# Kernel tuning notes

Hardware: AMD Instinct MI355X
Metric: run time of the kernel (lower is better)

Reference implementation:

```python
import jax, jax.numpy as jnp
import numpy as np
from jax import lax

B, S, D, STEPS, OUT = 512, 256, 256, 256, 3


def setup_inputs() -> dict:
    key = jax.random.key(0)
    ks = jax.random.split(key, 16)
    sc = 0.05
    n = lambda k, shp: jax.random.normal(k, shp, jnp.float32) * sc
    return {
        "e_all": jax.random.normal(ks[0], (B, S, D), jnp.float32),
        "e_last": jax.random.normal(ks[1], (1, B, D), jnp.float32),
        # NN_Attention params
        "Wa": n(ks[2], (D, D)), "ba": n(ks[3], (D,)),
        "Ua": n(ks[4], (D, D)), "bu": n(ks[5], (D,)),
        "Va": n(ks[6], (D,)), "bv": n(ks[7], ()),
        # GRU params (PyTorch layout: W_ih [3D, 3+D], W_hh [3D, D])
        "W_ih": n(ks[8], (3 * D, D + 3)), "b_ih": n(ks[9], (3 * D,)),
        "W_hh": n(ks[10], (3 * D, D)), "b_hh": n(ks[11], (3 * D,)),
        # output linear D -> 3
        "Wo": n(ks[12], (OUT, D)), "bo": n(ks[13], (OUT,)),
    }


def _decode(e_all, e_last, Wa, ba, Ua, bu, Va, bv, W_ih, b_ih, W_hh, b_hh, Wo, bo):
    # Ua(keys) is constant across steps -> precompute once (same math)
    Ua_keys = jnp.einsum('bsd,ed->bse', e_all, Ua) + bu  # [B, S, D]

    def step(carry, _):
        h, x_in = carry
        # Bahdanau attention: Va(tanh(Wa(q) + Ua(keys)))
        q = h @ Wa.T + ba                                       # [B, D]
        scores = jnp.einsum('bsd,d->bs', jnp.tanh(q[:, None, :] + Ua_keys), Va) + bv
        w = jax.nn.softmax(scores, axis=-1)                     # [B, S]
        ctx = jnp.einsum('bs,bsd->bd', w, e_all)                # [B, D]
        # GRU cell on input [context ; d_input] (cat order matches torch code)
        x = jnp.concatenate([ctx, x_in], axis=-1)               # [B, D+3]
        gi = x @ W_ih.T + b_ih
        gh = h @ W_hh.T + b_hh
        i_r, i_z, i_n = jnp.split(gi, 3, axis=-1)
        h_r, h_z, h_n = jnp.split(gh, 3, axis=-1)
        r = jax.nn.sigmoid(i_r + h_r)
        z = jax.nn.sigmoid(i_z + h_z)
        nn_ = jnp.tanh(i_n + r * h_n)
        h_new = (1.0 - z) * nn_ + z * h
        out = h_new @ Wo.T + bo                                 # [B, 3]
        return (h_new, out), (out, w)

    h0 = e_last[0]                                              # [B, D]
    x0 = jnp.zeros((h0.shape[0], OUT), h0.dtype)
    (hT, _), (outs, ws) = lax.scan(step, (h0, x0), None, length=STEPS)
    d_outputs = outs.transpose(1, 0, 2)                         # [B, STEPS, 3]
    cross_attn = ws.transpose(1, 0, 2).reshape(h0.shape[0], 1, STEPS * S)
    return d_outputs, hT[None], cross_attn


def reference(e_all, e_last, Wa, ba, Ua, bu, Va, bv, W_ih, b_ih, W_hh, b_hh, Wo, bo):
    return _decode(e_all, e_last, Wa, ba, Ua, bu, Va, bv, W_ih, b_ih, W_hh, b_hh, Wo, bo)
```

## Files before the change

kernel.cpp:

```cpp
#include <hip/hip_runtime.h>
#include <hip/hip_bf16.h>
#include <stdint.h>

#define NB 512
#define NS 256
#define ND 256
#define NT 256
#define NO 3

#define LOG2E 1.44269504088896340736f
#define C2 (2.0f*LOG2E)

typedef float f32x2 __attribute__((ext_vector_type(2)));

#if __has_builtin(__builtin_amdgcn_exp2f)
__device__ __forceinline__ float exp2_fast(float x){ return __builtin_amdgcn_exp2f(x); }
#else
__device__ __forceinline__ float exp2_fast(float x){ return exp2f(x); }
#endif
#if __has_builtin(__builtin_amdgcn_rcpf)
__device__ __forceinline__ float rcp_fast(float x){ return __builtin_amdgcn_rcpf(x); }
#else
__device__ __forceinline__ float rcp_fast(float x){ return 1.0f/x; }
#endif
// ... 100 lines not shown
  __shared__ float At[ND][20];
  const int t = threadIdx.x;
  const int m0 = blockIdx.x * 16;
  const int b  = m0 >> 8;
  const int s0 = m0 & (NS-1);
  #pragma unroll
  for (int i=0;i<16;i++)
    At[t][i] = e_all[(size_t)(m0+i)*ND + t];
  __syncthreads();
  float acc[16];
  float bue = bu[t];
  #pragma unroll
  for (int i=0;i<16;i++) acc[i] = bue;
  for (int d=0; d<ND; ++d){
    float u = UaT[d*ND + t];
    const float4 a0 = *(const float4*)&At[d][0];
    const float4 a1 = *(const float4*)&At[d][4];
    const float4 a2 = *(const float4*)&At[d][8];
    const float4 a3 = *(const float4*)&At[d][12];
    acc[0]+=a0.x*u;  acc[1]+=a0.y*u;  acc[2]+=a0.z*u;  acc[3]+=a0.w*u;
    acc[4]+=a1.x*u;  acc[5]+=a1.y*u;  acc[6]+=a1.z*u;  acc[7]+=a1.w*u;
    acc[8]+=a2.x*u;  acc[9]+=a2.y*u;  acc[10]+=a2.z*u; acc[11]+=a2.w*u;
    acc[12]+=a3.x*u; acc[13]+=a3.y*u; acc[14]+=a3.z*u; acc[15]+=a3.w*u;
  }
  const int e16 = t>>4, j = t&15;
  uint8_t* base = UKQ + (((size_t)b*16 + e16)*256 + s0)*16 + j;
  #pragma unroll
  for (int i=0;i<16;i++){
    uint32_t mine = enc_e4m3(acc[i] * C2);
    uint32_t other = (uint32_t)__shfl_xor((int)mine, 1);
    if (!(t & 1))
      *(uint16_t*)(base + (size_t)i*16) = (uint16_t)(mine | (other << 8));
  }
}

__global__ void k_epq(const float* __restrict__ e_all, uint32_t* __restrict__ EPQ){
  int idx = blockIdx.x*256 + threadIdx.x;
  if (idx >= NB*64*256) return;
  int d  = idx & 255;
  int s4 = (idx >> 8) & 63;
  int b  = idx >> 14;
  const float* e = e_all + ((size_t)b*NS + 4*s4)*ND + d;
  uint32_t v = (uint32_t)enc_e4m3(e[0])
             | ((uint32_t)enc_e4m3(e[ND])   << 8)
             | ((uint32_t)enc_e4m3(e[2*ND]) << 16)
             | ((uint32_t)enc_e4m3(e[3*ND]) << 24);
  EPQ[idx] = v;
}

__global__ void k_wh(const float* __restrict__ Wa, const float* __restrict__ W_hh,
                     uint4* __restrict__ WH){
  int idx = blockIdx.x*256 + threadIdx.x;
  if (idx >= 128*256) return;
  int d = idx & 255, k2 = idx >> 8;
  uint4 v;
  v.x = pack2(Wa  [(size_t)d*256       + 2*k2], Wa  [(size_t)d*256       + 2*k2+1]);
  v.y = pack2(W_hh[(size_t)d*256       + 2*k2], W_hh[(size_t)d*256       + 2*k2+1]);
  v.z = pack2(W_hh[(size_t)(256+d)*256 + 2*k2], W_hh[(size_t)(256+d)*256 + 2*k2+1]);
  v.w = pack2(W_hh[(size_t)(512+d)*256 + 2*k2], W_hh[(size_t)(512+d)*256 + 2*k2+1]);
  WH[idx] = v;
}

__global__ void k_wx(const float* __restrict__ W_ih, uint32_t* __restrict__ WX){
  int idx = blockIdx.x*256 + threadIdx.x;
  if (idx >= 132*256) return;
  int d = idx & 255, k2 = idx >> 8;
  float r0=0,r1=0,z0=0,z1=0,n0=0,n1=0;
  int ka = 2*k2, kb = 2*k2+1;
  if (ka < 259){
    r0 = W_ih[(size_t)d*259       + ka];
    z0 = W_ih[(size_t)(256+d)*259 + ka];
    n0 = W_ih[(size_t)(512+d)*259 + ka];
  }
  if (kb < 259){
    r1 = W_ih[(size_t)d*259       + kb];
    z1 = W_ih[(size_t)(256+d)*259 + kb];
    n1 = W_ih[(size_t)(512+d)*259 + kb];
  }
  WX[(size_t)idx*3+0] = pack2(r0,r1);
  WX[(size_t)idx*3+1] = pack2(z0,z1);
  WX[(size_t)idx*3+2] = pack2(n0,n1);
}

__global__ void __launch_bounds__(1024, 4) k_decode(
    const uint8_t* __restrict__ UKQ, const uint32_t* __restrict__ EPQ,
    const uint4* __restrict__ WH, const uint32_t* __restrict__ WX,
    const float* __restrict__ e_last,
    const float* __restrict__ Va, const float* __restrict__ bv,
    const float* __restrict__ b_ih, const float* __restrict__ b_hh,
    const float* __restrict__ ba, const float* __restrict__ bo,
    const float* __restrict__ Wo,
    float* __restrict__ dout, float* __restrict__ hT_out, float* __restrict__ ca)
{
  __shared__ __align__(16) uint8_t  ukl[65536];
  __shared__ __align__(16) uint32_t epl[16384];
  __shared__ __align__(16) float    scr[16][ND];
  __shared__ float    ghp[3][ND];
  __shared__ float    hf[ND];
  __shared__ float    xin[4];
  __shared__ uint32_t xb[260];
  __shared__ __align__(16) float qL[ND];
  __shared__ __align__(16) float va2[ND];
  __shared__ float    WoL[3*ND];
  __shared__ __align__(16) float wl[NS];
  __shared__ float    red[8];

  const int t    = threadIdx.x;
  const int d    = t & 255;
  const int q4   = t >> 8;
  const int lane = t & 63;
  const int w    = t >> 6;
  const int b0   = blockIdx.x * 2;

  if (q4 == 0){
    va2[d] = 2.0f*Va[d];
    WoL[d] = Wo[d]; WoL[256+d] = Wo[256+d]; WoL[512+d] = Wo[512+d];
  }
  const float bias_r  = b_ih[d]     + b_hh[d];
  const float bias_z  = b_ih[256+d] + b_hh[256+d];
  const float bias_ni = b_ih[512+d];
  const float bias_nh = b_hh[512+d];
  const float ba_d = ba[d];
  const float bv0  = bv[0];
  const float bo0 = bo[0], bo1 = bo[1], bo2 = bo[2];
  __syncthreads();
  float sumVaQ = 0.f;
  {
    #pragma unroll 8
    for (int e = q4*64; e < q4*64+64; ++e) sumVaQ += va2[e];
    sumVaQ *= 0.5f;
  }

  #pragma unroll 1
  for (int r=0; r<2; ++r){
    const int b = b0 + r;

    {
      const uint4* srcU = (const uint4*)(UKQ + (size_t)b*65536);
      uint4* dstU = (uint4*)ukl;
      #pragma unroll
      for (int i=0;i<4;i++) dstU[t + i*1024] = srcU[t + i*1024];
      const uint4* srcE = (const uint4*)(EPQ + (size_t)b*16384);
      uint4* dstE = (uint4*)epl;
      #pragma unroll
      for (int i=0;i<4;i++) dstE[t + i*1024] = srcE[t + i*1024];
    }
    if (q4 == 0){
      hf[d] = e_last[(size_t)b*ND + d];
      if (d < 4) xin[d] = 0.f;
    }
    __syncthreads();
    if (t < 128) xb[130+t] = pack2(hf[2*t], hf[2*t+1]);
    if (t == 128){ xb[128]=0u; xb[129]=0u; xb[258]=0u; xb[259]=0u; }
    __syncthreads();

    float* ca_b = ca   + (size_t)b*(NT*NS);
    float* do_b = dout + (size_t)b*(NT*NO);

    #pragma unroll 1
    for (int step=0; step<NT; ++step){
      {
        float aq=0.f, ar=0.f, az=0.f, an=0.f;
        const uint4* wh = WH + (size_t)(q4*32)*256 + d;
        const uint32_t* xh = &xb[130 + q4*32];
        #pragma unroll 1
        for (int kk=0; kk<32; kk+=4){
          uint4 w0 = wh[(size_t)(kk+0)*256];
          uint4 w1 = wh[(size_t)(kk+1)*256];
          uint4 w2 = wh[(size_t)(kk+2)*256];
          uint4 w3 = wh[(size_t)(kk+3)*256];
          uint32_t x0 = xh[kk+0], x1 = xh[kk+1], x2 = xh[kk+2], x3 = xh[kk+3];
          aq=dot2bf(w0.x,x0,aq); ar=dot2bf(w0.y,x0,ar); az=dot2bf(w0.z,x0,az); an=dot2bf(w0.w,x0,an);
          aq=dot2bf(w1.x,x1,aq); ar=dot2bf(w1.y,x1,ar); az=dot2bf(w1.z,x1,az); an=dot2bf(w1.w,x1,an);
          aq=dot2bf(w2.x,x2,aq); ar=dot2bf(w2.y,x2,ar); az=dot2bf(w2.z,x2,az); an=dot2bf(w2.w,x2,an);
          aq=dot2bf(w3.x,x3,aq); ar=dot2bf(w3.y,x3,ar); az=dot2bf(w3.z,x3,az); an=dot2bf(w3.w,x3,an);
        }
        scr[q4*4+0][d]=aq; scr[q4*4+1][d]=ar; scr[q4*4+2][d]=az; scr[q4*4+3][d]=an;
      }
      __syncthreads();
      if (q4 == 0){
        qL[d]     = ((scr[0][d]+scr[4][d]) + (scr[8][d]+scr[12][d]) + ba_d) * C2;
        ghp[0][d] =  (scr[1][d]+scr[5][d]) + (scr[9][d]+scr[13][d]);
        ghp[1][d] =  (scr[2][d]+scr[6][d]) + (scr[10][d]+scr[14][d]);
        ghp[2][d] =  (scr[3][d]+scr[7][d]) + (scr[11][d]+scr[15][d]);
      }
      __syncthreads();

      {
        float acc = 0.f;
        #pragma unroll
        for (int j=0;j<4;j++){
          uint4 u = *(const uint4*)(ukl + (size_t)(q4*4+j)*4096 + d*16);
          const float* qb = &qL[q4*64 + j*16];
          const float* vb = &va2[q4*64 + j*16];
          acc = s_dword(u.x, *(const float4*)&qb[0],  *(const float4*)&vb[0],  acc);
          acc = s_dword(u.y, *(const float4*)&qb[4],  *(const float4*)&vb[4],  acc);
          acc = s_dword(u.z, *(const float4*)&qb[8],  *(const float4*)&vb[8],  acc);
          acc = s_dword(u.w, *(const float4*)&qb[12], *(const float4*)&vb[12], acc);
        }
        scr[q4][d] = sumVaQ - acc;
      }
      __syncthreads();

      float p_reg = 0.f;
      if (q4 == 0){
        float sc = (scr[0][d]+scr[1][d]) + (scr[2][d]+scr[3][d]) + bv0;
        p_reg = exp2_fast(sc * LOG2E);
        float ssum = p_reg;
        #pragma unroll
        for (int o=32;o;o>>=1) ssum += __shfl_xor(ssum, o);
        if (lane==0) red[w] = ssum;
      }
      __syncthreads();
      if (q4 == 0){
        float ssum = (red[0]+red[1]) + (red[2]+red[3]);
        float wgt = p_reg * rcp_fast(ssum);
        __builtin_nontemporal_store(wgt, &ca_b[(size_t)step*NS + d]);
        wl[d] = wgt;
      }
      __syncthreads();

      {
        float c0=0,c1=0,c2=0,c3=0;
        #pragma unroll
        for (int i=0;i<4;i++){
          int s4 = w*4 + i;
          uint4 ev = *(const uint4*)(epl + (size_t)s4*256 + lane*4);
          float4 w4 = *(const float4*)&wl[s4*4];
          c0 = c_dword(ev.x, w4, c0);
          c1 = c_dword(ev.y, w4, c1);
          c2 = c_dword(ev.z, w4, c2);
          c3 = c_dword(ev.w, w4, c3);
        }
        *(float4*)&scr[w][lane*4] = make_float4(c0,c1,c2,c3);
      }
      __syncthreads();
      if (q4 == 0){
        float cx = 0.f;
        #pragma unroll
        for (int i=0;i<16;i++) cx += scr[i][d];
        float other = __shfl_xor(cx, 1);
        if (!(d&1)) xb[d>>1] = pack2(cx, other);
        if (d==128) xb[128] = pack2(xin[0], xin[1]);
        if (d==129) xb[129] = pack2(xin[2], 0.f);
      }
      __syncthreads();

      {
        float ar=0.f, az=0.f, an=0.f;
        const int k0 = q4*33;
        const uint32_t* wx = WX + ((size_t)k0*256 + d)*3;
        #pragma unroll 1
        for (int kk=0; kk<32; kk+=4){
          const uint32_t* p0 = wx + (size_t)(kk+0)*768;
          const uint32_t* p1 = wx + (size_t)(kk+1)*768;
          const uint32_t* p2 = wx + (size_t)(kk+2)*768;
          const uint32_t* p3 = wx + (size_t)(kk+3)*768;
          uint32_t r0=p0[0], z0=p0[1], n0=p0[2];
          uint32_t r1=p1[0], z1=p1[1], n1=p1[2];
          uint32_t r2=p2[0], z2=p2[1], n2=p2[2];
          uint32_t r3=p3[0], z3=p3[1], n3=p3[2];
          uint32_t x0 = xb[k0+kk+0], x1 = xb[k0+kk+1];
          uint32_t x2 = xb[k0+kk+2], x3 = xb[k0+kk+3];
          ar=dot2bf(r0,x0,ar); az=dot2bf(z0,x0,az); an=dot2bf(n0,x0,an);
          ar=dot2bf(r1,x1,ar); az=dot2bf(z1,x1,az); an=dot2bf(n1,x1,an);
          ar=dot2bf(r2,x2,ar); az=dot2bf(z2,x2,az); an=dot2bf(n2,x2,an);
          ar=dot2bf(r3,x3,ar); az=dot2bf(z3,x3,az); an=dot2bf(n3,x3,an);
        }
        {
          const uint32_t* p = wx + (size_t)32*768;
          uint32_t xa = xb[k0+32];
          ar=dot2bf(p[0],xa,ar); az=dot2bf(p[1],xa,az); an=dot2bf(p[2],xa,an);
        }
        scr[q4*3+0][d]=ar; scr[q4*3+1][d]=az; scr[q4*3+2][d]=an;
      }
      __syncthreads();
      if (q4 == 0){
        float ar  = (scr[0][d]+scr[3][d]) + (scr[6][d]+scr[9][d])  + ghp[0][d] + bias_r;
        float az  = (scr[1][d]+scr[4][d]) + (scr[7][d]+scr[10][d]) + ghp[1][d] + bias_z;
        float ani = (scr[2][d]+scr[5][d]) + (scr[8][d]+scr[11][d]) + bias_ni;
        float anh = ghp[2][d] + bias_nh;
        float rg = sigm_f(ar);
        float zg = sigm_f(az);
        float ng = tanh_f(ani + rg*anh);
        float hnew = (1.f-zg)*ng + zg*hf[d];
        hf[d] = hnew;
        float other = __shfl_xor(hnew, 1);
        if (!(d&1)) xb[130 + (d>>1)] = pack2(hnew, other);
      }
      __syncthreads();

      if (w == 0){
        float p0=0,p1=0,p2=0;
        #pragma unroll
        for (int i=0;i<4;i++){
          float hv = hf[i*64 + lane];
          p0 = fmaf(hv, WoL[      i*64+lane], p0);
          p1 = fmaf(hv, WoL[256 + i*64+lane], p1);
          p2 = fmaf(hv, WoL[512 + i*64+lane], p2);
        }
        #pragma unroll
        for (int o=32;o;o>>=1){
          p0+=__shfl_xor(p0,o); p1+=__shfl_xor(p1,o); p2+=__shfl_xor(p2,o);
        }
        if (lane==0){
          float o0=p0+bo0, o1=p1+bo1, o2=p2+bo2;
          __builtin_nontemporal_store(o0, &do_b[(size_t)step*NO+0]);
          __builtin_nontemporal_store(o1, &do_b[(size_t)step*NO+1]);
          __builtin_nontemporal_store(o2, &do_b[(size_t)step*NO+2]);
          xin[0]=o0; xin[1]=o1; xin[2]=o2;
        }
      }
    }

    __syncthreads();
    if (q4 == 0) hT_out[(size_t)b*ND + d] = hf[d];
    __syncthreads();
  }
}


extern "C" void kernel_launch(void* const* d_in, const int* in_sizes, int n_in,
                              void* d_out, int out_size, void* d_ws, size_t ws_size,
                              hipStream_t stream) {
  const float* e_all  = (const float*)d_in[0];
  const float* e_last = (const float*)d_in[1];
  const float* Wa     = (const float*)d_in[2];
  const float* ba     = (const float*)d_in[3];
  const float* Ua     = (const float*)d_in[4];
  const float* bu     = (const float*)d_in[5];
  const float* Va     = (const float*)d_in[6];
  const float* bv     = (const float*)d_in[7];
  const float* W_ih   = (const float*)d_in[8];
  const float* b_ih   = (const float*)d_in[9];
  const float* W_hh   = (const float*)d_in[10];
  const float* b_hh   = (const float*)d_in[11];
  const float* Wo     = (const float*)d_in[12];
  const float* bo     = (const float*)d_in[13];

  char* ws = (char*)d_ws;
  uint8_t*  UKQ = (uint8_t*) (ws + 0ull);
  uint32_t* EPQ = (uint32_t*)(ws + 33554432ull);
  uint4*    WH  = (uint4*)   (ws + 67108864ull);
  uint32_t* WX  = (uint32_t*)(ws + 67633152ull);
  float*    UaT = (float*)   (ws + 68038656ull);

  float* dout = (float*)d_out;
  float* hT   = dout + (size_t)NB*NT*NO;
  float* ca   = hT   + (size_t)NB*ND;

  k_transpose<<<(ND*ND+255)/256,256,0,stream>>>(Ua, UaT, ND, ND);
  k_uk<<<NB*NS/16,256,0,stream>>>(e_all, UaT, bu, UKQ);
  k_epq<<<(NB*64*256+255)/256,256,0,stream>>>(e_all, EPQ);
  k_wh<<<(128*256+255)/256,256,0,stream>>>(Wa, W_hh, WH);
  k_wx<<<(132*256+255)/256,256,0,stream>>>(W_ih, WX);

  k_decode<<<NB/2,1024,0,stream>>>(UKQ, EPQ, WH, WX, e_last, Va, bv,
                                   b_ih, b_hh, ba, bo, Wo, dout, hT, ca);
}
```

Baseline: 7.282 ms.

## Process both batch rows per block concurrently to share weight loads

```diff
diff --git a/kernel.cpp b/kernel.cpp
--- a/kernel.cpp
+++ b/kernel.cpp
@@ -216,17 +216,15 @@
     const float* __restrict__ Wo,
     float* __restrict__ dout, float* __restrict__ hT_out, float* __restrict__ ca)
 {
-  __shared__ __align__(16) uint8_t  ukl[65536];
-  __shared__ __align__(16) uint32_t epl[16384];
+  __shared__ __align__(16) uint8_t  ukl[131072];
   __shared__ __align__(16) float    scr[16][ND];
-  __shared__ float    ghp[3][ND];
-  __shared__ float    hf[ND];
-  __shared__ float    xin[4];
-  __shared__ uint32_t xb[260];
-  __shared__ __align__(16) float qL[ND];
+  __shared__ float    ghp[2][3][ND];
+  __shared__ float    hf[2][ND];
+  __shared__ float    xin[2][4];
+  __shared__ uint32_t xb[2][260];
+  __shared__ __align__(16) float qL[2][ND];
   __shared__ __align__(16) float va2[ND];
-  __shared__ float    WoL[3*ND];
-  __shared__ __align__(16) float wl[NS];
+  __shared__ __align__(16) float wl[2][NS];
   __shared__ float    red[8];
 
   const int t    = threadIdx.x;
@@ -235,10 +233,13 @@
   const int lane = t & 63;
   const int w    = t >> 6;
   const int b0   = blockIdx.x * 2;
-
-  if (q4 == 0){
-    va2[d] = 2.0f*Va[d];
-    WoL[d] = Wo[d]; WoL[256+d] = Wo[256+d]; WoL[512+d] = Wo[512+d];
+  const int bi   = q4 >> 1;
+  const int eh   = q4 & 1;
+
+  if (q4 == 0) va2[d] = 2.0f*Va[d];
+  if (q4 < 2){
+    hf[q4][d] = e_last[(size_t)(b0+q4)*ND + d];
+    if (d < 4) xin[q4][d] = 0.f;
   }
   const float bias_r  = b_ih[d]     + b_hh[d];
   const float bias_z  = b_ih[256+d] + b_hh[256+d];
@@ -247,200 +248,243 @@
   const float ba_d = ba[d];
   const float bv0  = bv[0];
   const float bo0 = bo[0], bo1 = bo[1], bo2 = bo[2];
+  float wo0[4], wo1[4], wo2[4];
+  if ((w & 7) == 0){
+    #pragma unroll
+    for (int i=0;i<4;i++){
+      wo0[i] = Wo[i*64+lane]; wo1[i] = Wo[256+i*64+lane]; wo2[i] = Wo[512+i*64+lane];
+    }
+  }
+  {
+    const uint4* srcU = (const uint4*)(UKQ + (size_t)b0*65536);
+    uint4* dstU = (uint4*)ukl;
+    #pragma unroll
+    for (int i=0;i<8;i++) dstU[t + i*1024] = srcU[t + i*1024];
+  }
   __syncthreads();
-  float sumVaQ = 0.f;
+  if (t < 256){
+    int bb = t>>7, i = t&127;
+    xb[bb][130+i] = pack2(hf[bb][2*i], hf[bb][2*i+1]);
+  }
+  if (t == 256){
+    xb[0][128]=0u; xb[0][129]=0u; xb[0][258]=0u; xb[0][259]=0u;
+    xb[1][128]=0u; xb[1][129]=0u; xb[1][258]=0u; xb[1][259]=0u;
+  }
+  float sumVaH = 0.f;
   {
     #pragma unroll 8
-    for (int e = q4*64; e < q4*64+64; ++e) sumVaQ += va2[e];
-    sumVaQ *= 0.5f;
-  }
+    for (int e = eh*128; e < eh*128+128; ++e) sumVaH += va2[e];
+    sumVaH *= 0.5f;
+  }
+  __syncthreads();
+
+  const uint8_t* ukb = ukl + ((size_t)(bi*16 + eh*8)*256 + d)*16;
 
   #pragma unroll 1
-  for (int r=0; r<2; ++r){
-    const int b = b0 + r;
-
+  for (int step=0; step<NT; ++step){
+    float a0q=0,a0r=0,a0z=0,a0n=0, a1q=0,a1r=0,a1z=0,a1n=0;
     {
-      const uint4* srcU = (const uint4*)(UKQ + (size_t)b*65536);
-      uint4* dstU = (uint4*)ukl;
+      const uint4* wh = WH + (size_t)(q4*32)*256 + d;
+      const uint32_t* xh0 = &xb[0][130 + q4*32];
+      const uint32_t* xh1 = &xb[1][130 + q4*32];
+      #pragma unroll 1
+      for (int kk=0; kk<32; kk+=4){
+        uint4 w0 = wh[(size_t)(kk+0)*256];
+        uint4 w1 = wh[(size_t)(kk+1)*256];
+        uint4 w2 = wh[(size_t)(kk+2)*256];
+        uint4 w3 = wh[(size_t)(kk+3)*256];
+        uint32_t x00=xh0[kk+0], x01=xh0[kk+1], x02=xh0[kk+2], x03=xh0[kk+3];
+        uint32_t x10=xh1[kk+0], x11=xh1[kk+1], x12=xh1[kk+2], x13=xh1[kk+3];
+        a0q=dot2bf(w0.x,x00,a0q); a0r=dot2bf(w0.y,x00,a0r); a0z=dot2bf(w0.z,x00,a0z); a0n=dot2bf(w0.w,x00,a0n);
+        a1q=dot2bf(w0.x,x10,a1q); a1r=dot2bf(w0.y,x10,a1r); a1z=dot2bf(w0.z,x10,a1z); a1n=dot2bf(w0.w,x10,a1n);
+        a0q=dot2bf(w1.x,x01,a0q); a0r=dot2bf(w1.y,x01,a0r); a0z=dot2bf(w1.z,x01,a0z); a0n=dot2bf(w1.w,x01,a0n);
+        a1q=dot2bf(w1.x,x11,a1q); a1r=dot2bf(w1.y,x11,a1r); a1z=dot2bf(w1.z,x11,a1z); a1n=dot2bf(w1.w,x11,a1n);
+        a0q=dot2bf(w2.x,x02,a0q); a0r=dot2bf(w2.y,x02,a0r); a0z=dot2bf(w2.z,x02,a0z); a0n=dot2bf(w2.w,x02,a0n);
+        a1q=dot2bf(w2.x,x12,a1q); a1r=dot2bf(w2.y,x12,a1r); a1z=dot2bf(w2.z,x12,a1z); a1n=dot2bf(w2.w,x12,a1n);
+        a0q=dot2bf(w3.x,x03,a0q); a0r=dot2bf(w3.y,x03,a0r); a0z=dot2bf(w3.z,x03,a0z); a0n=dot2bf(w3.w,x03,a0n);
+        a1q=dot2bf(w3.x,x13,a1q); a1r=dot2bf(w3.y,x13,a1r); a1z=dot2bf(w3.z,x13,a1z); a1n=dot2bf(w3.w,x13,a1n);
+      }
+    }
+    if (q4 < 2){
+      scr[ 0+q4][d]=a0q; scr[ 2+q4][d]=a0r; scr[ 4+q4][d]=a0z; scr[ 6+q4][d]=a0n;
+      scr[ 8+q4][d]=a1q; scr[10+q4][d]=a1r; scr[12+q4][d]=a1z; scr[14+q4][d]=a1n;
+    }
+    __syncthreads();
+    if (q4 >= 2){
+      const int ph = q4 & 1;
+      scr[ 0+ph][d]+=a0q; scr[ 2+ph][d]+=a0r; scr[ 4+ph][d]+=a0z; scr[ 6+ph][d]+=a0n;
+      scr[ 8+ph][d]+=a1q; scr[10+ph][d]+=a1r; scr[12+ph][d]+=a1z; scr[14+ph][d]+=a1n;
+    }
+    __syncthreads();
+    if (q4 < 2){
+      const int rb = q4*8;
+      qL[q4][d]     = (scr[rb+0][d]+scr[rb+1][d] + ba_d) * C2;
+      ghp[q4][0][d] =  scr[rb+2][d]+scr[rb+3][d];
+      ghp[q4][1][d] =  scr[rb+4][d]+scr[rb+5][d];
+      ghp[q4][2][d] =  scr[rb+6][d]+scr[rb+7][d];
+    }
+    __syncthreads();
+
+    {
+      float acc = 0.f;
       #pragma unroll
-      for (int i=0;i<4;i++) dstU[t + i*1024] = srcU[t + i*1024];
-      const uint4* srcE = (const uint4*)(EPQ + (size_t)b*16384);
-      uint4* dstE = (uint4*)epl;
+      for (int j=0;j<8;j++){
+        uint4 u = *(const uint4*)(ukb + (size_t)j*4096);
+        const float* qb = &qL[bi][eh*128 + j*16];
+        const float* vb = &va2[eh*128 + j*16];
+        acc = s_dword(u.x, *(const float4*)&qb[0],  *(const float4*)&vb[0],  acc);
+        acc = s_dword(u.y, *(const float4*)&qb[4],  *(const float4*)&vb[4],  acc);
+        acc = s_dword(u.z, *(const float4*)&qb[8],  *(const float4*)&vb[8],  acc);
+        acc = s_dword(u.w, *(const float4*)&qb[12], *(const float4*)&vb[12], acc);
+      }
+      scr[q4][d] = sumVaH - acc;
+    }
+    __syncthreads();
+
+    float p_reg = 0.f;
+    if (q4 < 2){
+      float sc = scr[q4*2+0][d] + scr[q4*2+1][d] + bv0;
+      p_reg = exp2_fast(sc * LOG2E);
+      float ssum = p_reg;
       #pragma unroll
-      for (int i=0;i<4;i++) dstE[t + i*1024] = srcE[t + i*1024];
-    }
-    if (q4 == 0){
-      hf[d] = e_last[(size_t)b*ND + d];
-      if (d < 4) xin[d] = 0.f;
-    }
-    __syncthreads();
-    if (t < 128) xb[130+t] = pack2(hf[2*t], hf[2*t+1]);
-    if (t == 128){ xb[128]=0u; xb[129]=0u; xb[258]=0u; xb[259]=0u; }
-    __syncthreads();
-
-    float* ca_b = ca   + (size_t)b*(NT*NS);
-    float* do_b = dout + (size_t)b*(NT*NO);
-
-    #pragma unroll 1
-    for (int step=0; step<NT; ++step){
+      for (int o=32;o;o>>=1) ssum += __shfl_xor(ssum, o);
+      if (lane==0) red[w] = ssum;
+    }
+    __syncthreads();
+    if (q4 < 2){
+      const int rb = q4*4;
+      float ssum = (red[rb]+red[rb+1]) + (red[rb+2]+red[rb+3]);
+      float wgt = p_reg * rcp_fast(ssum);
+      float* ca_b = ca + (size_t)(b0+q4)*(NT*NS);
+      __builtin_nontemporal_store(wgt, &ca_b[(size_t)step*NS + d]);
+      wl[q4][d] = wgt;
+    }
+    __syncthreads();
+
+    {
+      const int cb = w>>3, sub = w&7;
+      const uint32_t* epb = EPQ + (size_t)(b0+cb)*16384;
+      float c0=0,c1=0,c2=0,c3=0;
+      #pragma unroll
+      for (int gq=0; gq<2; ++gq){
+        const int s40 = sub*8 + gq*4;
+        uint4 e0v = *(const uint4*)(epb + (size_t)(s40+0)*256 + lane*4);
+        uint4 e1v = *(const uint4*)(epb + (size_t)(s40+1)*256 + lane*4);
+        uint4 e2v = *(const uint4*)(epb + (size_t)(s40+2)*256 + lane*4);
+        uint4 e3v = *(const uint4*)(epb + (size_t)(s40+3)*256 + lane*4);
+        float4 w40 = *(const float4*)&wl[cb][(s40+0)*4];
+        c0=c_dword(e0v.x,w40,c0); c1=c_dword(e0v.y,w40,c1);
+        c2=c_dword(e0v.z,w40,c2); c3=c_dword(e0v.w,w40,c3);
+        float4 w41 = *(const float4*)&wl[cb][(s40+1)*4];
+        c0=c_dword(e1v.x,w41,c0); c1=c_dword(e1v.y,w41,c1);
+        c2=c_dword(e1v.z,w41,c2); c3=c_dword(e1v.w,w41,c3);
+        float4 w42 = *(const float4*)&wl[cb][(s40+2)*4];
+        c0=c_dword(e2v.x,w42,c0); c1=c_dword(e2v.y,w42,c1);
+        c2=c_dword(e2v.z,w42,c2); c3=c_dword(e2v.w,w42,c3);
+        float4 w43 = *(const float4*)&wl[cb][(s40+3)*4];
+        c0=c_dword(e3v.x,w43,c0); c1=c_dword(e3v.y,w43,c1);
+        c2=c_dword(e3v.z,w43,c2); c3=c_dword(e3v.w,w43,c3);
+      }
+      *(float4*)&scr[w][lane*4] = make_float4(c0,c1,c2,c3);
+    }
+    __syncthreads();
+    if (q4 < 2){
+      float cx = 0.f;
+      #pragma unroll
+      for (int i=0;i<8;i++) cx += scr[q4*8+i][d];
+      float other = __shfl_xor(cx, 1);
+      if (!(d&1)) xb[q4][d>>1] = pack2(cx, other);
+      if (d==128) xb[q4][128] = pack2(xin[q4][0], xin[q4][1]);
+      if (d==129) xb[q4][129] = pack2(xin[q4][2], 0.f);
+    }
+    __syncthreads();
+
+    float d0r=0,d0z=0,d0n=0, d1r=0,d1z=0,d1n=0;
+    {
+      const int k0 = q4*33;
+      const uint32_t* wx = WX + ((size_t)k0*256 + d)*3;
+      #pragma unroll 1
+      for (int kk=0; kk<32; kk+=4){
+        const uint32_t* p0 = wx + (size_t)(kk+0)*768;
+        const uint32_t* p1 = wx + (size_t)(kk+1)*768;
+        const uint32_t* p2 = wx + (size_t)(kk+2)*768;
+        const uint32_t* p3 = wx + (size_t)(kk+3)*768;
+        uint32_t r0=p0[0], z0=p0[1], n0=p0[2];
+        uint32_t r1=p1[0], z1=p1[1], n1=p1[2];
+        uint32_t r2=p2[0], z2=p2[1], n2=p2[2];
+        uint32_t r3=p3[0], z3=p3[1], n3=p3[2];
+        uint32_t x00=xb[0][k0+kk+0], x01=xb[0][k0+kk+1], x02=xb[0][k0+kk+2], x03=xb[0][k0+kk+3];
+        uint32_t x10=xb[1][k0+kk+0], x11=xb[1][k0+kk+1], x12=xb[1][k0+kk+2], x13=xb[1][k0+kk+3];
+        d0r=dot2bf(r0,x00,d0r); d0z=dot2bf(z0,x00,d0z); d0n=dot2bf(n0,x00,d0n);
+        d1r=dot2bf(r0,x10,d1r); d1z=dot2bf(z0,x10,d1z); d1n=dot2bf(n0,x10,d1n);
+        d0r=dot2bf(r1,x01,d0r); d0z=dot2bf(z1,x01,d0z); d0n=dot2bf(n1,x01,d0n);
+        d1r=dot2bf(r1,x11,d1r); d1z=dot2bf(z1,x11,d1z); d1n=dot2bf(n1,x11,d1n);
+        d0r=dot2bf(r2,x02,d0r); d0z=dot2bf(z2,x02,d0z); d0n=dot2bf(n2,x02,d0n);
+        d1r=dot2bf(r2,x12,d1r); d1z=dot2bf(z2,x12,d1z); d1n=dot2bf(n2,x12,d1n);
+        d0r=dot2bf(r3,x03,d0r); d0z=dot2bf(z3,x03,d0z); d0n=dot2bf(n3,x03,d0n);
+        d1r=dot2bf(r3,x13,d1r); d1z=dot2bf(z3,x13,d1z); d1n=dot2bf(n3,x13,d1n);
+      }
       {
-        float aq=0.f, ar=0.f, az=0.f, an=0.f;
-        const uint4* wh = WH + (size_t)(q4*32)*256 + d;
-        const uint32_t* xh = &xb[130 + q4*32];
-        #pragma unroll 1
-        for (int kk=0; kk<32; kk+=4){
-          uint4 w0 = wh[(size_t)(kk+0)*256];
-          uint4 w1 = wh[(size_t)(kk+1)*256];
-          uint4 w2 = wh[(size_t)(kk+2)*256];
-          uint4 w3 = wh[(size_t)(kk+3)*256];
-          uint32_t x0 = xh[kk+0], x1 = xh[kk+1], x2 = xh[kk+2], x3 = xh[kk+3];
-          aq=dot2bf(w0.x,x0,aq); ar=dot2bf(w0.y,x0,ar); az=dot2bf(w0.z,x0,az); an=dot2bf(w0.w,x0,an);
-          aq=dot2bf(w1.x,x1,aq); ar=dot2bf(w1.y,x1,ar); az=dot2bf(w1.z,x1,az); an=dot2bf(w1.w,x1,an);
-          aq=dot2bf(w2.x,x2,aq); ar=dot2bf(w2.y,x2,ar); az=dot2bf(w2.z,x2,az); an=dot2bf(w2.w,x2,an);
-          aq=dot2bf(w3.x,x3,aq); ar=dot2bf(w3.y,x3,ar); az=dot2bf(w3.z,x3,az); an=dot2bf(w3.w,x3,an);
-        }
-        scr[q4*4+0][d]=aq; scr[q4*4+1][d]=ar; scr[q4*4+2][d]=az; scr[q4*4+3][d]=an;
-      }
-      __syncthreads();
-      if (q4 == 0){
-        qL[d]     = ((scr[0][d]+scr[4][d]) + (scr[8][d]+scr[12][d]) + ba_d) * C2;
-        ghp[0][d] =  (scr[1][d]+scr[5][d]) + (scr[9][d]+scr[13][d]);
-        ghp[1][d] =  (scr[2][d]+scr[6][d]) + (scr[10][d]+scr[14][d]);
-        ghp[2][d] =  (scr[3][d]+scr[7][d]) + (scr[11][d]+scr[15][d]);
-      }
-      __syncthreads();
-
-      {
-        float acc = 0.f;
-        #pragma unroll
-        for (int j=0;j<4;j++){
-          uint4 u = *(const uint4*)(ukl + (size_t)(q4*4+j)*4096 + d*16);
-          const float* qb = &qL[q4*64 + j*16];
-          const float* vb = &va2[q4*64 + j*16];
-          acc = s_dword(u.x, *(const float4*)&qb[0],  *(const float4*)&vb[0],  acc);
-          acc = s_dword(u.y, *(const float4*)&qb[4],  *(const float4*)&vb[4],  acc);
-          acc = s_dword(u.z, *(const float4*)&qb[8],  *(const float4*)&vb[8],  acc);
-          acc = s_dword(u.w, *(const float4*)&qb[12], *(const float4*)&vb[12], acc);
-        }
-        scr[q4][d] = sumVaQ - acc;
-      }
-      __syncthreads();
-
-      float p_reg = 0.f;
-      if (q4 == 0){
-        float sc = (scr[0][d]+scr[1][d]) + (scr[2][d]+scr[3][d]) + bv0;
-        p_reg = exp2_fast(sc * LOG2E);
-        float ssum = p_reg;
-        #pragma unroll
-        for (int o=32;o;o>>=1) ssum += __shfl_xor(ssum, o);
-        if (lane==0) red[w] = ssum;
-      }
-      __syncthreads();
-      if (q4 == 0){
-        float ssum = (red[0]+red[1]) + (red[2]+red[3]);
-        float wgt = p_reg * rcp_fast(ssum);
-        __builtin_nontemporal_store(wgt, &ca_b[(size_t)step*NS + d]);
-        wl[d] = wgt;
-      }
-      __syncthreads();
-
-      {
-        float c0=0,c1=0,c2=0,c3=0;
-        #pragma unroll
-        for (int i=0;i<4;i++){
-          int s4 = w*4 + i;
-          uint4 ev = *(const uint4*)(epl + (size_t)s4*256 + lane*4);
-          float4 w4 = *(const float4*)&wl[s4*4];
-          c0 = c_dword(ev.x, w4, c0);
-          c1 = c_dword(ev.y, w4, c1);
-          c2 = c_dword(ev.z, w4, c2);
-          c3 = c_dword(ev.w, w4, c3);
-        }
-        *(float4*)&scr[w][lane*4] = make_float4(c0,c1,c2,c3);
-      }
-      __syncthreads();
-      if (q4 == 0){
-        float cx = 0.f;
-        #pragma unroll
-        for (int i=0;i<16;i++) cx += scr[i][d];
-        float other = __shfl_xor(cx, 1);
-        if (!(d&1)) xb[d>>1] = pack2(cx, other);
-        if (d==128) xb[128] = pack2(xin[0], xin[1]);
-        if (d==129) xb[129] = pack2(xin[2], 0.f);
-      }
-      __syncthreads();
-
-      {
-        float ar=0.f, az=0.f, an=0.f;
-        const int k0 = q4*33;
-        const uint32_t* wx = WX + ((size_t)k0*256 + d)*3;
-        #pragma unroll 1
-        for (int kk=0; kk<32; kk+=4){
-          const uint32_t* p0 = wx + (size_t)(kk+0)*768;
-          const uint32_t* p1 = wx + (size_t)(kk+1)*768;
-          const uint32_t* p2 = wx + (size_t)(kk+2)*768;
-          const uint32_t* p3 = wx + (size_t)(kk+3)*768;
-          uint32_t r0=p0[0], z0=p0[1], n0=p0[2];
-          uint32_t r1=p1[0], z1=p1[1], n1=p1[2];
-          uint32_t r2=p2[0], z2=p2[1], n2=p2[2];
-          uint32_t r3=p3[0], z3=p3[1], n3=p3[2];
-          uint32_t x0 = xb[k0+kk+0], x1 = xb[k0+kk+1];
-          uint32_t x2 = xb[k0+kk+2], x3 = xb[k0+kk+3];
-          ar=dot2bf(r0,x0,ar); az=dot2bf(z0,x0,az); an=dot2bf(n0,x0,an);
-          ar=dot2bf(r1,x1,ar); az=dot2bf(z1,x1,az); an=dot2bf(n1,x1,an);
-          ar=dot2bf(r2,x2,ar); az=dot2bf(z2,x2,az); an=dot2bf(n2,x2,an);
-          ar=dot2bf(r3,x3,ar); az=dot2bf(z3,x3,az); an=dot2bf(n3,x3,an);
-        }
-        {
-          const uint32_t* p = wx + (size_t)32*768;
-          uint32_t xa = xb[k0+32];
-          ar=dot2bf(p[0],xa,ar); az=dot2bf(p[1],xa,az); an=dot2bf(p[2],xa,an);
-        }
-        scr[q4*3+0][d]=ar; scr[q4*3+1][d]=az; scr[q4*3+2][d]=an;
-      }
-      __syncthreads();
-      if (q4 == 0){
-        float ar  = (scr[0][d]+scr[3][d]) + (scr[6][d]+scr[9][d])  + ghp[0][d] + bias_r;
-        float az  = (scr[1][d]+scr[4][d]) + (scr[7][d]+scr[10][d]) + ghp[1][d] + bias_z;
-        float ani = (scr[2][d]+scr[5][d]) + (scr[8][d]+scr[11][d]) + bias_ni;
-        float anh = ghp[2][d] + bias_nh;
-        float rg = sigm_f(ar);
-        float zg = sigm_f(az);
-        float ng = tanh_f(ani + rg*anh);
-        float hnew = (1.f-zg)*ng + zg*hf[d];
-        hf[d] = hnew;
-        float other = __shfl_xor(hnew, 1);
-        if (!(d&1)) xb[130 + (d>>1)] = pack2(hnew, other);
-      }
-      __syncthreads();
-
-      if (w == 0){
-        float p0=0,p1=0,p2=0;
-        #pragma unroll
-        for (int i=0;i<4;i++){
-          float hv = hf[i*64 + lane];
-          p0 = fmaf(hv, WoL[      i*64+lane], p0);
-          p1 = fmaf(hv, WoL[256 + i*64+lane], p1);
-          p2 = fmaf(hv, WoL[512 + i*64+lane], p2);
-        }
-        #pragma unroll
-        for (int o=32;o;o>>=1){
-          p0+=__shfl_xor(p0,o); p1+=__shfl_xor(p1,o); p2+=__shfl_xor(p2,o);
-        }
-        if (lane==0){
-          float o0=p0+bo0, o1=p1+bo1, o2=p2+bo2;
-          __builtin_nontemporal_store(o0, &do_b[(size_t)step*NO+0]);
-          __builtin_nontemporal_store(o1, &do_b[(size_t)step*NO+1]);
-          __builtin_nontemporal_store(o2, &do_b[(size_t)step*NO+2]);
-          xin[0]=o0; xin[1]=o1; xin[2]=o2;
-        }
-      }
-    }
-
-    __syncthreads();
-    if (q4 == 0) hT_out[(size_t)b*ND + d] = hf[d];
-    __syncthreads();
-  }
+        const uint32_t* p = wx + (size_t)32*768;
+        uint32_t xa = xb[0][k0+32], xc = xb[1][k0+32];
+        d0r=dot2bf(p[0],xa,d0r); d0z=dot2bf(p[1],xa,d0z); d0n=dot2bf(p[2],xa,d0n);
+        d1r=dot2bf(p[0],xc,d1r); d1z=dot2bf(p[1],xc,d1z); d1n=dot2bf(p[2],xc,d1n);
+      }
+    }
+    if (q4 < 2){
+      scr[ 0+q4][d]=d0r; scr[ 2+q4][d]=d0z; scr[ 4+q4][d]=d0n;
+      scr[ 6+q4][d]=d1r; scr[ 8+q4][d]=d1z; scr[10+q4][d]=d1n;
+    }
+    __syncthreads();
+    if (q4 >= 2){
+      const int ph = q4 & 1;
+      scr[ 0+ph][d]+=d0r; scr[ 2+ph][d]+=d0z; scr[ 4+ph][d]+=d0n;
+      scr[ 6+ph][d]+=d1r; scr[ 8+ph][d]+=d1z; scr[10+ph][d]+=d1n;
+    }
+    __syncthreads();
+    if (q4 < 2){
+      const int rb = q4*6;
+      float ar  = scr[rb+0][d]+scr[rb+1][d] + ghp[q4][0][d] + bias_r;
+      float az  = scr[rb+2][d]+scr[rb+3][d] + ghp[q4][1][d] + bias_z;
+      float ani = scr[rb+4][d]+scr[rb+5][d] + bias_ni;
+      float anh = ghp[q4][2][d] + bias_nh;
+      float rg = sigm_f(ar);
+      float zg = sigm_f(az);
+      float ng = tanh_f(ani + rg*anh);
+      float hnew = (1.f-zg)*ng + zg*hf[q4][d];
+      hf[q4][d] = hnew;
+      float other = __shfl_xor(hnew, 1);
+      if (!(d&1)) xb[q4][130 + (d>>1)] = pack2(hnew, other);
+    }
+    __syncthreads();
+
+    if ((w & 7) == 0){
+      const int bq = w >> 3;
+      float p0=0,p1=0,p2=0;
+      #pragma unroll
+      for (int i=0;i<4;i++){
+        float hv = hf[bq][i*64 + lane];
+        p0 = fmaf(hv, wo0[i], p0);
+        p1 = fmaf(hv, wo1[i], p1);
+        p2 = fmaf(hv, wo2[i], p2);
+      }
+      #pragma unroll
+      for (int o=32;o;o>>=1){
+        p0+=__shfl_xor(p0,o); p1+=__shfl_xor(p1,o); p2+=__shfl_xor(p2,o);
+      }
+      if (lane==0){
+        float o0=p0+bo0, o1=p1+bo1, o2=p2+bo2;
+        float* do_b = dout + (size_t)(b0+bq)*(NT*NO);
+        __builtin_nontemporal_store(o0, &do_b[(size_t)step*NO+0]);
+        __builtin_nontemporal_store(o1, &do_b[(size_t)step*NO+1]);
+        __builtin_nontemporal_store(o2, &do_b[(size_t)step*NO+2]);
+        xin[bq][0]=o0; xin[bq][1]=o1; xin[bq][2]=o2;
+      }
+    }
+  }
+
+  __syncthreads();
+  if (q4 < 2) hT_out[(size_t)(b0+q4)*ND + d] = hf[q4][d];
 }
 
 
```

New measurement: 9.313 ms. 27.9% more time.

## Use one 512-thread block per batch row with encoder values held in registers

Applied to the files above, without the earlier changes.

```diff
diff --git a/kernel.cpp b/kernel.cpp
--- a/kernel.cpp
+++ b/kernel.cpp
@@ -206,7 +206,7 @@
   WX[(size_t)idx*3+2] = pack2(n0,n1);
 }
 
-__global__ void __launch_bounds__(1024, 4) k_decode(
+__global__ void __launch_bounds__(512, 4) k_decode(
     const uint8_t* __restrict__ UKQ, const uint32_t* __restrict__ EPQ,
     const uint4* __restrict__ WH, const uint32_t* __restrict__ WX,
     const float* __restrict__ e_last,
@@ -217,28 +217,24 @@
     float* __restrict__ dout, float* __restrict__ hT_out, float* __restrict__ ca)
 {
   __shared__ __align__(16) uint8_t  ukl[65536];
-  __shared__ __align__(16) uint32_t epl[16384];
-  __shared__ __align__(16) float    scr[16][ND];
-  __shared__ float    ghp[3][ND];
+  __shared__ __align__(16) float    scr[11][ND];
+  __shared__ __align__(16) float    va2[ND];
+  __shared__ __align__(16) float    wl[NS];
   __shared__ float    hf[ND];
+  __shared__ uint32_t xb[258];
   __shared__ float    xin[4];
-  __shared__ uint32_t xb[260];
-  __shared__ __align__(16) float qL[ND];
-  __shared__ __align__(16) float va2[ND];
-  __shared__ float    WoL[3*ND];
-  __shared__ __align__(16) float wl[NS];
-  __shared__ float    red[8];
 
   const int t    = threadIdx.x;
   const int d    = t & 255;
-  const int q4   = t >> 8;
+  const int half = t >> 8;
   const int lane = t & 63;
   const int w    = t >> 6;
-  const int b0   = blockIdx.x * 2;
-
-  if (q4 == 0){
+  const int b    = blockIdx.x;
+
+  if (half == 0){
     va2[d] = 2.0f*Va[d];
-    WoL[d] = Wo[d]; WoL[256+d] = Wo[256+d]; WoL[512+d] = Wo[512+d];
+    hf[d]  = e_last[(size_t)b*ND + d];
+    if (d < 4) xin[d] = 0.f;
   }
   const float bias_r  = b_ih[d]     + b_hh[d];
   const float bias_z  = b_ih[256+d] + b_hh[256+d];
@@ -247,200 +243,174 @@
   const float ba_d = ba[d];
   const float bv0  = bv[0];
   const float bo0 = bo[0], bo1 = bo[1], bo2 = bo[2];
+  {
+    const uint4* srcU = (const uint4*)(UKQ + (size_t)b*65536);
+    uint4* dstU = (uint4*)ukl;
+    #pragma unroll
+    for (int i=0;i<8;i++) dstU[t + i*512] = srcU[t + i*512];
+  }
+  uint4 ep[8];
+  {
+    const uint32_t* epb = EPQ + (size_t)b*16384;
+    #pragma unroll
+    for (int i=0;i<8;i++)
+      ep[i] = *(const uint4*)(epb + (size_t)(w*8+i)*256 + lane*4);
+  }
   __syncthreads();
-  float sumVaQ = 0.f;
+  if (t < 128) xb[130+t] = pack2(hf[2*t], hf[2*t+1]);
+  if (t == 128){ xb[128]=0u; xb[129]=0u; }
+  float sumVaH = 0.f;
   {
     #pragma unroll 8
-    for (int e = q4*64; e < q4*64+64; ++e) sumVaQ += va2[e];
-    sumVaQ *= 0.5f;
-  }
+    for (int e = half*128; e < half*128+128; ++e) sumVaH += va2[e];
+    sumVaH *= 0.5f;
+  }
+  __syncthreads();
+
+  float* ca_b = ca   + (size_t)b*(NT*NS);
+  float* do_b = dout + (size_t)b*(NT*NO);
 
   #pragma unroll 1
-  for (int r=0; r<2; ++r){
-    const int b = b0 + r;
-
+  for (int step=0; step<NT; ++step){
     {
-      const uint4* srcU = (const uint4*)(UKQ + (size_t)b*65536);
-      uint4* dstU = (uint4*)ukl;
-      #pragma unroll
-      for (int i=0;i<4;i++) dstU[t + i*1024] = srcU[t + i*1024];
-      const uint4* srcE = (const uint4*)(EPQ + (size_t)b*16384);
-      uint4* dstE = (uint4*)epl;
-      #pragma unroll
-      for (int i=0;i<4;i++) dstE[t + i*1024] = srcE[t + i*1024];
-    }
-    if (q4 == 0){
-      hf[d] = e_last[(size_t)b*ND + d];
-      if (d < 4) xin[d] = 0.f;
-    }
-    __syncthreads();
-    if (t < 128) xb[130+t] = pack2(hf[2*t], hf[2*t+1]);
-    if (t == 128){ xb[128]=0u; xb[129]=0u; xb[258]=0u; xb[259]=0u; }
-    __syncthreads();
-
-    float* ca_b = ca   + (size_t)b*(NT*NS);
-    float* do_b = dout + (size_t)b*(NT*NO);
-
-    #pragma unroll 1
-    for (int step=0; step<NT; ++step){
-      {
-        float aq=0.f, ar=0.f, az=0.f, an=0.f;
-        const uint4* wh = WH + (size_t)(q4*32)*256 + d;
-        const uint32_t* xh = &xb[130 + q4*32];
-        #pragma unroll 1
-        for (int kk=0; kk<32; kk+=4){
-          uint4 w0 = wh[(size_t)(kk+0)*256];
-          uint4 w1 = wh[(size_t)(kk+1)*256];
-          uint4 w2 = wh[(size_t)(kk+2)*256];
-          uint4 w3 = wh[(size_t)(kk+3)*256];
-          uint32_t x0 = xh[kk+0], x1 = xh[kk+1], x2 = xh[kk+2], x3 = xh[kk+3];
-          aq=dot2bf(w0.x,x0,aq); ar=dot2bf(w0.y,x0,ar); az=dot2bf(w0.z,x0,az); an=dot2bf(w0.w,x0,an);
-          aq=dot2bf(w1.x,x1,aq); ar=dot2bf(w1.y,x1,ar); az=dot2bf(w1.z,x1,az); an=dot2bf(w1.w,x1,an);
-          aq=dot2bf(w2.x,x2,aq); ar=dot2bf(w2.y,x2,ar); az=dot2bf(w2.z,x2,az); an=dot2bf(w2.w,x2,an);
-          aq=dot2bf(w3.x,x3,aq); ar=dot2bf(w3.y,x3,ar); az=dot2bf(w3.z,x3,az); an=dot2bf(w3.w,x3,an);
-        }
-        scr[q4*4+0][d]=aq; scr[q4*4+1][d]=ar; scr[q4*4+2][d]=az; scr[q4*4+3][d]=an;
-      }
-      __syncthreads();
-      if (q4 == 0){
-        qL[d]     = ((scr[0][d]+scr[4][d]) + (scr[8][d]+scr[12][d]) + ba_d) * C2;
-        ghp[0][d] =  (scr[1][d]+scr[5][d]) + (scr[9][d]+scr[13][d]);
-        ghp[1][d] =  (scr[2][d]+scr[6][d]) + (scr[10][d]+scr[14][d]);
-        ghp[2][d] =  (scr[3][d]+scr[7][d]) + (scr[11][d]+scr[15][d]);
-      }
-      __syncthreads();
-
-      {
-        float acc = 0.f;
-        #pragma unroll
-        for (int j=0;j<4;j++){
-          uint4 u = *(const uint4*)(ukl + (size_t)(q4*4+j)*4096 + d*16);
-          const float* qb = &qL[q4*64 + j*16];
-          const float* vb = &va2[q4*64 + j*16];
-          acc = s_dword(u.x, *(const float4*)&qb[0],  *(const float4*)&vb[0],  acc);
-          acc = s_dword(u.y, *(const float4*)&qb[4],  *(const float4*)&vb[4],  acc);
-          acc = s_dword(u.z, *(const float4*)&qb[8],  *(const float4*)&vb[8],  acc);
-          acc = s_dword(u.w, *(const float4*)&qb[12], *(const float4*)&vb[12], acc);
-        }
-        scr[q4][d] = sumVaQ - acc;
-      }
-      __syncthreads();
-
-      float p_reg = 0.f;
-      if (q4 == 0){
-        float sc = (scr[0][d]+scr[1][d]) + (scr[2][d]+scr[3][d]) + bv0;
-        p_reg = exp2_fast(sc * LOG2E);
-        float ssum = p_reg;
-        #pragma unroll
-        for (int o=32;o;o>>=1) ssum += __shfl_xor(ssum, o);
-        if (lane==0) red[w] = ssum;
-      }
-      __syncthreads();
-      if (q4 == 0){
-        float ssum = (red[0]+red[1]) + (red[2]+red[3]);
-        float wgt = p_reg * rcp_fast(ssum);
-        __builtin_nontemporal_store(wgt, &ca_b[(size_t)step*NS + d]);
-        wl[d] = wgt;
-      }
-      __syncthreads();
-
-      {
-        float c0=0,c1=0,c2=0,c3=0;
-        #pragma unroll
-        for (int i=0;i<4;i++){
-          int s4 = w*4 + i;
-          uint4 ev = *(const uint4*)(epl + (size_t)s4*256 + lane*4);
-          float4 w4 = *(const float4*)&wl[s4*4];
-          c0 = c_dword(ev.x, w4, c0);
-          c1 = c_dword(ev.y, w4, c1);
-          c2 = c_dword(ev.z, w4, c2);
-          c3 = c_dword(ev.w, w4, c3);
-        }
-        *(float4*)&scr[w][lane*4] = make_float4(c0,c1,c2,c3);
-      }
-      __syncthreads();
-      if (q4 == 0){
-        float cx = 0.f;
-        #pragma unroll
-        for (int i=0;i<16;i++) cx += scr[i][d];
-        float other = __shfl_xor(cx, 1);
-        if (!(d&1)) xb[d>>1] = pack2(cx, other);
-        if (d==128) xb[128] = pack2(xin[0], xin[1]);
-        if (d==129) xb[129] = pack2(xin[2], 0.f);
-      }
-      __syncthreads();
-
-      {
-        float ar=0.f, az=0.f, an=0.f;
-        const int k0 = q4*33;
-        const uint32_t* wx = WX + ((size_t)k0*256 + d)*3;
-        #pragma unroll 1
-        for (int kk=0; kk<32; kk+=4){
-          const uint32_t* p0 = wx + (size_t)(kk+0)*768;
-          const uint32_t* p1 = wx + (size_t)(kk+1)*768;
-          const uint32_t* p2 = wx + (size_t)(kk+2)*768;
-          const uint32_t* p3 = wx + (size_t)(kk+3)*768;
-          uint32_t r0=p0[0], z0=p0[1], n0=p0[2];
-          uint32_t r1=p1[0], z1=p1[1], n1=p1[2];
-          uint32_t r2=p2[0], z2=p2[1], n2=p2[2];
-          uint32_t r3=p3[0], z3=p3[1], n3=p3[2];
-          uint32_t x0 = xb[k0+kk+0], x1 = xb[k0+kk+1];
-          uint32_t x2 = xb[k0+kk+2], x3 = xb[k0+kk+3];
-          ar=dot2bf(r0,x0,ar); az=dot2bf(z0,x0,az); an=dot2bf(n0,x0,an);
-          ar=dot2bf(r1,x1,ar); az=dot2bf(z1,x1,az); an=dot2bf(n1,x1,an);
-          ar=dot2bf(r2,x2,ar); az=dot2bf(z2,x2,az); an=dot2bf(n2,x2,an);
-          ar=dot2bf(r3,x3,ar); az=dot2bf(z3,x3,az); an=dot2bf(n3,x3,an);
-        }
-        {
-          const uint32_t* p = wx + (size_t)32*768;
-          uint32_t xa = xb[k0+32];
-          ar=dot2bf(p[0],xa,ar); az=dot2bf(p[1],xa,az); an=dot2bf(p[2],xa,an);
-        }
-        scr[q4*3+0][d]=ar; scr[q4*3+1][d]=az; scr[q4*3+2][d]=an;
-      }
-      __syncthreads();
-      if (q4 == 0){
-        float ar  = (scr[0][d]+scr[3][d]) + (scr[6][d]+scr[9][d])  + ghp[0][d] + bias_r;
-        float az  = (scr[1][d]+scr[4][d]) + (scr[7][d]+scr[10][d]) + ghp[1][d] + bias_z;
-        float ani = (scr[2][d]+scr[5][d]) + (scr[8][d]+scr[11][d]) + bias_ni;
-        float anh = ghp[2][d] + bias_nh;
-        float rg = sigm_f(ar);
-        float zg = sigm_f(az);
-        float ng = tanh_f(ani + rg*anh);
-        float hnew = (1.f-zg)*ng + zg*hf[d];
-        hf[d] = hnew;
-        float other = __shfl_xor(hnew, 1);
-        if (!(d&1)) xb[130 + (d>>1)] = pack2(hnew, other);
-      }
-      __syncthreads();
-
-      if (w == 0){
-        float p0=0,p1=0,p2=0;
-        #pragma unroll
-        for (int i=0;i<4;i++){
-          float hv = hf[i*64 + lane];
-          p0 = fmaf(hv, WoL[      i*64+lane], p0);
-          p1 = fmaf(hv, WoL[256 + i*64+lane], p1);
-          p2 = fmaf(hv, WoL[512 + i*64+lane], p2);
-        }
-        #pragma unroll
-        for (int o=32;o;o>>=1){
-          p0+=__shfl_xor(p0,o); p1+=__shfl_xor(p1,o); p2+=__shfl_xor(p2,o);
-        }
-        if (lane==0){
-          float o0=p0+bo0, o1=p1+bo1, o2=p2+bo2;
-          __builtin_nontemporal_store(o0, &do_b[(size_t)step*NO+0]);
-          __builtin_nontemporal_store(o1, &do_b[(size_t)step*NO+1]);
-          __builtin_nontemporal_store(o2, &do_b[(size_t)step*NO+2]);
-          xin[0]=o0; xin[1]=o1; xin[2]=o2;
-        }
-      }
-    }
-
-    __syncthreads();
-    if (q4 == 0) hT_out[(size_t)b*ND + d] = hf[d];
-    __syncthreads();
-  }
+      float aq=0.f, ar_=0.f, az_=0.f, an_=0.f;
+      const uint4* wh = WH + (size_t)(half*64)*256 + d;
+      const uint32_t* xh = &xb[130 + half*64];
+      #pragma unroll 1
+      for (int kk=0; kk<64; kk+=2){
+        uint4 w0 = wh[(size_t)(kk+0)*256];
+        uint4 w1 = wh[(size_t)(kk+1)*256];
+        uint32_t x0 = xh[kk+0], x1 = xh[kk+1];
+        aq =dot2bf(w0.x,x0,aq);  ar_=dot2bf(w0.y,x0,ar_);
+        az_=dot2bf(w0.z,x0,az_); an_=dot2bf(w0.w,x0,an_);
+        aq =dot2bf(w1.x,x1,aq);  ar_=dot2bf(w1.y,x1,ar_);
+        az_=dot2bf(w1.z,x1,az_); an_=dot2bf(w1.w,x1,an_);
+      }
+      scr[0+half][d]=aq; scr[2+half][d]=ar_; scr[4+half][d]=az_; scr[6+half][d]=an_;
+    }
+    __syncthreads();
+    if (half == 0){
+      float ql   = (scr[0][d]+scr[1][d] + ba_d) * C2;
+      scr[8][d]  =  scr[2][d]+scr[3][d];
+      scr[9][d]  =  scr[4][d]+scr[5][d];
+      scr[10][d] =  scr[6][d]+scr[7][d];
+      scr[2][d]  =  ql;
+    }
+    __syncthreads();
+
+    {
+      float acc = 0.f;
+      #pragma unroll
+      for (int j=0;j<8;j++){
+        uint4 u = *(const uint4*)(ukl + (size_t)(((half*8+j)*256 + d) << 4));
+        const float* qb = &scr[2][half*128 + j*16];
+        const float* vb = &va2[half*128 + j*16];
+        acc = s_dword(u.x, *(const float4*)&qb[0],  *(const float4*)&vb[0],  acc);
+        acc = s_dword(u.y, *(const float4*)&qb[4],  *(const float4*)&vb[4],  acc);
+        acc = s_dword(u.z, *(const float4*)&qb[8],  *(const float4*)&vb[8],  acc);
+        acc = s_dword(u.w, *(const float4*)&qb[12], *(const float4*)&vb[12], acc);
+      }
+      scr[half][d] = sumVaH - acc;
+    }
+    __syncthreads();
+
+    float p_reg = 0.f;
+    if (half == 0){
+      float sc = scr[0][d] + scr[1][d] + bv0;
+      p_reg = exp2_fast(sc * LOG2E);
+      float ssum = p_reg;
+      #pragma unroll
+      for (int o=32;o;o>>=1) ssum += __shfl_xor(ssum, o);
+      if (lane==0) scr[3][w] = ssum;
+    }
+    __syncthreads();
+    if (half == 0){
+      float ssum = (scr[3][0]+scr[3][1]) + (scr[3][2]+scr[3][3]);
+      float wgt = p_reg * rcp_fast(ssum);
+      __builtin_nontemporal_store(wgt, &ca_b[(size_t)step*NS + d]);
+      wl[d] = wgt;
+    }
+    __syncthreads();
+
+    {
+      float c0=0,c1=0,c2=0,c3=0;
+      #pragma unroll
+      for (int i=0;i<8;i++){
+        const float4 w4 = *(const float4*)&wl[(w*8+i)*4];
+        c0 = c_dword(ep[i].x, w4, c0);
+        c1 = c_dword(ep[i].y, w4, c1);
+        c2 = c_dword(ep[i].z, w4, c2);
+        c3 = c_dword(ep[i].w, w4, c3);
+      }
+      *(float4*)&scr[w][lane*4] = make_float4(c0,c1,c2,c3);
+    }
+    __syncthreads();
+    if (half == 0){
+      float cx = 0.f;
+      #pragma unroll
+      for (int i=0;i<8;i++) cx += scr[i][d];
+      float other = __shfl_xor(cx, 1);
+      if (!(d&1)) xb[d>>1] = pack2(cx, other);
+      if (d==128) xb[128] = pack2(xin[0], xin[1]);
+      if (d==129) xb[129] = pack2(xin[2], 0.f);
+    }
+    __syncthreads();
+
+    {
+      float dr=0.f, dz=0.f, dn=0.f;
+      const int k0 = half*66;
+      const uint32_t* wx = WX + ((size_t)k0*256 + d)*3;
+      #pragma unroll 1
+      for (int kk=0; kk<66; kk+=2){
+        const uint32_t* p0 = wx + (size_t)(kk+0)*768;
+        const uint32_t* p1 = wx + (size_t)(kk+1)*768;
+        uint32_t x0 = xb[k0+kk+0], x1 = xb[k0+kk+1];
+        dr=dot2bf(p0[0],x0,dr); dz=dot2bf(p0[1],x0,dz); dn=dot2bf(p0[2],x0,dn);
+        dr=dot2bf(p1[0],x1,dr); dz=dot2bf(p1[1],x1,dz); dn=dot2bf(p1[2],x1,dn);
+      }
+      scr[0+half][d]=dr; scr[2+half][d]=dz; scr[4+half][d]=dn;
+    }
+    __syncthreads();
+    if (half == 0){
+      float ar  = scr[0][d]+scr[1][d] + scr[8][d] + bias_r;
+      float az  = scr[2][d]+scr[3][d] + scr[9][d] + bias_z;
+      float ani = scr[4][d]+scr[5][d] + bias_ni;
+      float anh = scr[10][d] + bias_nh;
+      float rg = sigm_f(ar);
+      float zg = sigm_f(az);
+      float ng = tanh_f(ani + rg*anh);
+      float hnew = (1.f-zg)*ng + zg*hf[d];
+      hf[d] = hnew;
+      float other = __shfl_xor(hnew, 1);
+      if (!(d&1)) xb[130 + (d>>1)] = pack2(hnew, other);
+    }
+    __syncthreads();
+
+    if (w == 0){
+      float p0=0,p1=0,p2=0;
+      #pragma unroll
+      for (int i=0;i<4;i++){
+        float hv = hf[i*64 + lane];
+        p0 = fmaf(hv, Wo[      i*64+lane], p0);
+        p1 = fmaf(hv, Wo[256 + i*64+lane], p1);
+        p2 = fmaf(hv, Wo[512 + i*64+lane], p2);
+      }
+      #pragma unroll
+      for (int o=32;o;o>>=1){
+        p0+=__shfl_xor(p0,o); p1+=__shfl_xor(p1,o); p2+=__shfl_xor(p2,o);
+      }
+      if (lane==0){
+        float o0=p0+bo0, o1=p1+bo1, o2=p2+bo2;
+        __builtin_nontemporal_store(o0, &do_b[(size_t)step*NO+0]);
+        __builtin_nontemporal_store(o1, &do_b[(size_t)step*NO+1]);
+        __builtin_nontemporal_store(o2, &do_b[(size_t)step*NO+2]);
+        xin[0]=o0; xin[1]=o1; xin[2]=o2;
+      }
+    }
+  }
+
+  __syncthreads();
+  if (half == 0) hT_out[(size_t)b*ND + d] = hf[d];
 }
 
 
@@ -479,6 +449,6 @@
   k_wh<<<(128*256+255)/256,256,0,stream>>>(Wa, W_hh, WH);
   k_wx<<<(132*256+255)/256,256,0,stream>>>(W_ih, WX);
 
-  k_decode<<<NB/2,1024,0,stream>>>(UKQ, EPQ, WH, WX, e_last, Va, bv,
-                                   b_ih, b_hh, ba, bo, Wo, dout, hT, ca);
-}
+  k_decode<<<NB,512,0,stream>>>(UKQ, EPQ, WH, WX, e_last, Va, bv,
+                                b_ih, b_hh, ba, bo, Wo, dout, hT, ca);
+}
```

After: 11.88 ms. +63.1%, slower.
